# Optimization experiments

Hardware: AMD Instinct MI355X
Metric: run time of the kernel (lower is better)

The kernel has to match this reference:

```python
import jax, jax.numpy as jnp
import numpy as np

N, M, D = 2048, 50000, 128


def setup_inputs() -> dict:
    key = jax.random.key(0)
    kz, kr = jax.random.split(key)
    z = jax.random.normal(kz, (N, D), dtype=jnp.float32)
    ref = jax.random.normal(kr, (M, D), dtype=jnp.float32)  # stands in for the concatenated in_dl batches
    return {"z": z, "ref": ref, "k": 10}


def reference(z, ref, k):
    # L2-normalize rows (matches z / z.norm(dim=1, keepdim=True))
    zn = z / jnp.linalg.norm(z, axis=1, keepdims=True)      # [N, D]
    rn = ref / jnp.linalg.norm(ref, axis=1, keepdims=True)  # [M, D]
    # Pairwise L2 distances via ||a||^2 + ||b||^2 - 2 a.b (same math as the
    # broadcast (rep_batch - rep_z).norm(dim=2), without the O(N*M*D) blowup).
    sq = (jnp.sum(zn * zn, axis=1)[:, None]
          + jnp.sum(rn * rn, axis=1)[None, :]
          - 2.0 * jnp.einsum('nd,md->nm', zn, rn))          # [N, M]
    dist = jnp.sqrt(jnp.maximum(sq, 1e-12))
    # Full sort along the reference axis, take the k-th smallest distance.
    return jnp.sort(dist, axis=1)[:, k]                      # [N]
```

## Files before the change

kernel.cpp:

```cpp
#include <hip/hip_runtime.h>


#define D_DIM 128
#define TQB 256
#define BR 64
#define NCH 64
#define NSUB (NCH * 32)
#define KK 11
#define NCAND 32
#define SLOTS 26
#define DNF 2816

typedef __bf16 bf16_t;
typedef bf16_t bf16x8 __attribute__((ext_vector_type(8)));
typedef float f32x16 __attribute__((ext_vector_type(16)));

__device__ __forceinline__ unsigned short f2bf(float f) {
    unsigned u = __float_as_uint(f);
    return (unsigned short)((u + 0x7fffu + ((u >> 16) & 1u)) >> 16);
}

__global__ __launch_bounds__(256) void normalize_bf16(
    const float* __restrict__ z, const float* __restrict__ ref,
    unsigned short* __restrict__ zb, unsigned short* __restrict__ rb,
    int N, int M)
{
    const int w = threadIdx.x >> 6;
    const int l = threadIdx.x & 63;
    const int row = blockIdx.x * 4 + w;
    if (row >= N + M) return;
    const float* in; unsigned short* out; int r;
    if (row < N) { in = z;   out = zb; r = row; }
    else         { in = ref; out = rb; r = row - N; }
    const float2 v = ((const float2*)in)[(size_t)r * 64 + l];
    float ss = v.x * v.x + v.y * v.y;
    #pragma unroll
    for (int off = 32; off > 0; off >>= 1) ss += __shfl_xor(ss, off);
    const float inv = rsqrtf(ss);
    ushort2 o; o.x = f2bf(v.x * inv); o.y = f2bf(v.y * inv);
    ((ushort2*)out)[(size_t)r * 64 + l] = o;
}

__device__ __forceinline__ void gld_lds16(const unsigned short* g,
                                          unsigned short* l) {
    __builtin_amdgcn_global_load_lds(
        (__attribute__((address_space(1))) void*)g,
        (__attribute__((address_space(3))) void*)l, 16, 0, 0);
}

__global__ __launch_bounds__(512) void knn_maxes(
    const unsigned short* __restrict__ zb, const unsigned short* __restrict__ rb,
    float* __restrict__ maxes, int N, int M, int chunk)
{
    __shared__ __align__(16) unsigned short Bt[2 * BR * D_DIM];

    const int nwg = 8 * NCH;
    const int bid = (int)blockIdx.x + 8 * (int)blockIdx.y;
    const int swz = (bid & 7) * (nwg >> 3) + (bid >> 3);
    const int bx = swz & 7;
    const int by = swz >> 3;

    const int t = threadIdx.x;
    const int lane = t & 63;
    const int w = t >> 6;
    const int quad = lane >> 4;
    const int ln = lane & 15;
    const int l31 = lane & 31;
    const int hi = lane >> 5;
    const int row = bx * TQB + w * 32 + l31;
    const int c0 = by * chunk;
    const int c1 = min(c0 + chunk, M);
    const int clen = c1 - c0;
    const int nt = (clen + BR - 1) / BR;

    bf16x8 qfr[8];
    #pragma unroll
    for (int ks = 0; ks < 8; ++ks)
        qfr[ks] = *(const bf16x8*)&zb[(size_t)row * D_DIM + ks * 16 + hi * 8];

    float mx[16];
    #pragma unroll
    for (int r = 0; r < 16; ++r) mx[r] = -3.0f;

    auto stage = [&](int half, int tile) {
        const int s0 = c0 + tile * BR;
        #pragma unroll
        for (int i = 0; i < 2; ++i) {
            const int r = w * 8 + i * 4 + quad;
            int g = s0 + r; if (g > M - 1) g = M - 1;
            const int sl = ln ^ (r & 15);
            gld_lds16(&rb[(size_t)g * D_DIM + sl * 8],
                      &Bt[half * (BR * D_DIM) + (w * 8 + i * 4) * D_DIM]);
        }
    };

    stage(0, 0);
    stage(1, nt > 1 ? 1 : 0);

    for (int it = 0; it < nt; ++it) {
        if (it + 1 < nt) asm volatile("s_waitcnt vmcnt(2)" ::: "memory");
        else             asm volatile("s_waitcnt vmcnt(0)" ::: "memory");
        __builtin_amdgcn_s_barrier();
        asm volatile("" ::: "memory");
        __builtin_amdgcn_sched_barrier(0);

        const int cur = it & 1;
        const unsigned short* Bc = &Bt[cur * (BR * D_DIM)];

        f32x16 acc0 = {0,0,0,0,0,0,0,0,0,0,0,0,0,0,0,0};
        f32x16 acc1 = {0,0,0,0,0,0,0,0,0,0,0,0,0,0,0,0};

        __builtin_amdgcn_s_setprio(1);
        #pragma unroll
        for (int ks = 0; ks < 8; ++ks) {
            const int sl = ((ks * 2 + hi) ^ ln) * 8;
            bf16x8 a0 = *(const bf16x8*)&Bc[(l31)      * D_DIM + sl];
            bf16x8 a1 = *(const bf16x8*)&Bc[(32 + l31) * D_DIM + sl];
            acc0 = __builtin_amdgcn_mfma_f32_32x32x16_bf16(a0, qfr[ks], acc0, 0, 0, 0);
            acc1 = __builtin_amdgcn_mfma_f32_32x32x16_bf16(a1, qfr[ks], acc1, 0, 0, 0);
        }
        __builtin_amdgcn_s_setprio(0);

        const int rem = clen - it * BR;
        if (rem >= BR) {
            #pragma unroll
            for (int r = 0; r < 16; ++r)
                mx[r] = fmaxf(mx[r], fmaxf(acc0[r], acc1[r]));
        } else {
            #pragma unroll
            for (int r = 0; r < 16; ++r) {
                const int crow = (r & 3) + 8 * (r >> 2) + 4 * hi;
                if (crow < rem)      mx[r] = fmaxf(mx[r], acc0[r]);
                if (32 + crow < rem) mx[r] = fmaxf(mx[r], acc1[r]);
            }
        }

        __builtin_amdgcn_sched_barrier(0);
        asm volatile("" ::: "memory");
        __builtin_amdgcn_s_barrier();
        if (it + 2 < nt) stage(cur, it + 2);
    }

    float* mp = &maxes[(size_t)row * NSUB + by * 32 + hi * 16];
    #pragma unroll
    for (int r4 = 0; r4 < 4; ++r4) {
        float4 v4 = { mx[r4 * 4], mx[r4 * 4 + 1], mx[r4 * 4 + 2], mx[r4 * 4 + 3] };
        *(float4*)&mp[r4 * 4] = v4;
    }
}

__device__ __forceinline__ float kth_largest_64(float* s, int kk, int t) {
    float cur = -3.0f;
    for (int it = 0; it <= kk; ++it) {
        float m = s[0];
        #pragma unroll
        for (int off = 32; off > 0; off >>= 1) m = fmaxf(m, __shfl_xor(m, off));
        cur = m;
        unsigned long long b = __ballot(s[0] == m);
        bool owner = ((int)(__ffsll(b) - 1) == t);
        #pragma unroll
        for (int j = 0; j < KK - 1; ++j) s[j] = owner ? s[j + 1] : s[j];
        if (owner) s[KK - 1] = -3.0f;
    }
    return cur;
}

__global__ __launch_bounds__(256) void knn_select(
    const unsigned short* __restrict__ zb, const unsigned short* __restrict__ rb,
    const float* __restrict__ maxes, const int* __restrict__ kp,
    float* __restrict__ out, int M, int chunk)
{
    const int row = blockIdx.x;
    const int t = threadIdx.x;
    __shared__ float dbuf[DNF];
    __shared__ int cand_s[NCAND];
    __shared__ int cn_s;

    const int kk = *kp;
    if (t == 0) cn_s = 0;

    if (t < 64) {
        float s[KK];
        #pragma unroll
        for (int j = 0; j < KK; ++j) s[j] = -3.0f;
        #pragma unroll
        for (int i = 0; i < NSUB / 64; ++i) {
            float v = maxes[(size_t)row * NSUB + t + 64 * i];
            #pragma unroll
            for (int j = 0; j < KK; ++j) {
                float hi = fmaxf(s[j], v), lo = fminf(s[j], v);
                s[j] = hi; v = lo;
            }
        }
        const float T = kth_largest_64(s, kk, t);
        #pragma unroll
        for (int i = 0; i < NSUB / 64; ++i) {
            float v = maxes[(size_t)row * NSUB + t + 64 * i];
            if (v >= T) {
                int sl = atomicAdd(&cn_s, 1);
                if (sl < NCAND) cand_s[sl] = t + 64 * i;
            }
        }
    }

    const int gl = t & 7;
    const int grp = t >> 3;
    float q0r[8], q1r[8];
    {
        bf16x8 qv0 = *(const bf16x8*)&zb[(size_t)row * D_DIM + gl * 8];
        bf16x8 qv1 = *(const bf16x8*)&zb[(size_t)row * D_DIM + 64 + gl * 8];
        #pragma unroll
        for (int e = 0; e < 8; ++e) { q0r[e] = (float)qv0[e]; q1r[e] = (float)qv1[e]; }
    }
    __syncthreads();

    const int cn = cn_s;
    const int slots = ((chunk + 63) >> 6) * 2;
    int nsel;

    if (cn <= NCAND && slots <= SLOTS) {
        const int W = cn * slots;
        for (int i = t; i < W; i += 256) dbuf[i] = -3.0f;
        __syncthreads();
        for (int ci = 0; ci < cn; ++ci) {
            const int s  = cand_s[ci];
            const int by = s >> 5;
            const int h2 = (s >> 4) & 1;
            const int r  = s & 15;
            const int base = (r & 3) + 8 * (r >> 2) + 4 * h2;
            const int c0 = by * chunk;
            const int c1 = min(c0 + chunk, M);
            for (int sl = grp; sl < slots; sl += 32) {
                const int ref = c0 + (sl >> 1) * 64 + (sl & 1) * 32 + base;
                const bool valid = ref < c1;
                float p = 0.f;
                if (valid) {
                    const unsigned short* rp = &rb[(size_t)ref * D_DIM + gl * 8];
                    bf16x8 r0 = *(const bf16x8*)rp;
                    bf16x8 r1 = *(const bf16x8*)(rp + 64);
                    #pragma unroll
                    for (int e = 0; e < 8; ++e) {
                        p = fmaf((float)r0[e], q0r[e], p);
                        p = fmaf((float)r1[e], q1r[e], p);
                    }
                }
                p += __shfl_xor(p, 1);
                p += __shfl_xor(p, 2);
                p += __shfl_xor(p, 4);
                if (gl == 0 && valid) dbuf[ci * slots + sl] = p;
            }
        }
        nsel = W;
    } else {
        float s[KK];
        #pragma unroll
        for (int j = 0; j < KK; ++j) s[j] = -3.0f;
        for (int g = grp; g < M; g += 32) {
            const unsigned short* rp = &rb[(size_t)g * D_DIM + gl * 8];
            bf16x8 r0 = *(const bf16x8*)rp;
            bf16x8 r1 = *(const bf16x8*)(rp + 64);
            float p = 0.f;
            #pragma unroll
            for (int e = 0; e < 8; ++e) {
                p = fmaf((float)r0[e], q0r[e], p);
                p = fmaf((float)r1[e], q1r[e], p);
            }
            p += __shfl_xor(p, 1);
            p += __shfl_xor(p, 2);
            p += __shfl_xor(p, 4);
            #pragma unroll
            for (int j = 0; j < KK; ++j) {
                float hi = fmaxf(s[j], p), lo = fminf(s[j], p);
                s[j] = hi; p = lo;
            }
        }
        #pragma unroll
        for (int j = 0; j < KK; ++j) dbuf[t * KK + j] = s[j];
        nsel = DNF;
    }
    __syncthreads();

    if (t < 64) {
        float s[KK];
        #pragma unroll
        for (int j = 0; j < KK; ++j) s[j] = -3.0f;
        for (int j = t; j < nsel; j += 64) {
            float v = dbuf[j];
            #pragma unroll
            for (int q = 0; q < KK; ++q) {
                float hi = fmaxf(s[q], v), lo = fminf(s[q], v);
                s[q] = hi; v = lo;
            }
        }
        const float cur = kth_largest_64(s, kk, t);
        if (t == 0) out[row] = sqrtf(fmaxf(2.0f - 2.0f * cur, 1e-12f));
    }
}

extern "C" void kernel_launch(void* const* d_in, const int* in_sizes, int n_in,
                              void* d_out, int out_size, void* d_ws, size_t ws_size,
                              hipStream_t stream) {
    const float* z   = (const float*)d_in[0];
    const float* ref = (const float*)d_in[1];
    const int*   kp  = (const int*)d_in[2];
    float* out = (float*)d_out;

    const int N = in_sizes[0] / D_DIM;
    const int M = in_sizes[1] / D_DIM;

    unsigned short* zbuf = (unsigned short*)d_ws;
    unsigned short* rbuf = zbuf + (size_t)N * D_DIM;
    float* maxes = (float*)(rbuf + (size_t)M * D_DIM);

    normalize_bf16<<<(N + M + 3) / 4, 256, 0, stream>>>(z, ref, zbuf, rbuf, N, M);

    const int chunk = (M + NCH - 1) / NCH;
    dim3 grid(N / TQB, NCH);

    knn_maxes<<<grid, 512, 0, stream>>>(zbuf, rbuf, maxes, N, M, chunk);
    knn_select<<<N, 256, 0, stream>>>(zbuf, rbuf, maxes, kp, out, M, chunk);
}
```

Baseline: 137.4 us.

## Double ref tile to 128 rows and parallelize candidate selection across four waves

The ref tile per pipeline stage in knn_maxes grows from 64 to 128 rows, using four MFMA accumulators per wave and an occupancy hint of two blocks per CU. This halves the number of barrier/wait iterations per chunk at the cost of more LDS and registers. In knn_select, the top-k threshold over the maxes array is now computed by all four waves, each producing a partial top-k that is merged by one wave. The candidate rescoring loop is flattened across candidates and slots, which removes a separate zero-fill pass and keeps the thread groups busy.

```diff
diff --git a/kernel.cpp b/kernel.cpp
--- a/kernel.cpp
+++ b/kernel.cpp
@@ -3,12 +3,12 @@
 
 #define D_DIM 128
 #define TQB 256
-#define BR 64
+#define BR 128
 #define NCH 64
 #define NSUB (NCH * 32)
 #define KK 11
 #define NCAND 32
-#define SLOTS 26
+#define SLOTS 28
 #define DNF 2816
 
 typedef __bf16 bf16_t;
@@ -48,7 +48,7 @@
         (__attribute__((address_space(3))) void*)l, 16, 0, 0);
 }
 
-__global__ __launch_bounds__(512) void knn_maxes(
+__global__ __launch_bounds__(512, 2) void knn_maxes(
     const unsigned short* __restrict__ zb, const unsigned short* __restrict__ rb,
     float* __restrict__ maxes, int N, int M, int chunk)
 {
@@ -85,12 +85,12 @@
     auto stage = [&](int half, int tile) {
         const int s0 = c0 + tile * BR;
         #pragma unroll
-        for (int i = 0; i < 2; ++i) {
-            const int r = w * 8 + i * 4 + quad;
+        for (int i = 0; i < 4; ++i) {
+            const int r = w * 16 + i * 4 + quad;
             int g = s0 + r; if (g > M - 1) g = M - 1;
             const int sl = ln ^ (r & 15);
             gld_lds16(&rb[(size_t)g * D_DIM + sl * 8],
-                      &Bt[half * (BR * D_DIM) + (w * 8 + i * 4) * D_DIM]);
+                      &Bt[half * (BR * D_DIM) + (w * 16 + i * 4) * D_DIM]);
         }
     };
 
@@ -98,7 +98,7 @@
     stage(1, nt > 1 ? 1 : 0);
 
     for (int it = 0; it < nt; ++it) {
-        if (it + 1 < nt) asm volatile("s_waitcnt vmcnt(2)" ::: "memory");
+        if (it + 1 < nt) asm volatile("s_waitcnt vmcnt(4)" ::: "memory");
         else             asm volatile("s_waitcnt vmcnt(0)" ::: "memory");
         __builtin_amdgcn_s_barrier();
         asm volatile("" ::: "memory");
@@ -109,6 +109,8 @@
 
         f32x16 acc0 = {0,0,0,0,0,0,0,0,0,0,0,0,0,0,0,0};
         f32x16 acc1 = {0,0,0,0,0,0,0,0,0,0,0,0,0,0,0,0};
+        f32x16 acc2 = {0,0,0,0,0,0,0,0,0,0,0,0,0,0,0,0};
+        f32x16 acc3 = {0,0,0,0,0,0,0,0,0,0,0,0,0,0,0,0};
 
         __builtin_amdgcn_s_setprio(1);
         #pragma unroll
@@ -116,8 +118,12 @@
             const int sl = ((ks * 2 + hi) ^ ln) * 8;
             bf16x8 a0 = *(const bf16x8*)&Bc[(l31)      * D_DIM + sl];
             bf16x8 a1 = *(const bf16x8*)&Bc[(32 + l31) * D_DIM + sl];
+            bf16x8 a2 = *(const bf16x8*)&Bc[(64 + l31) * D_DIM + sl];
+            bf16x8 a3 = *(const bf16x8*)&Bc[(96 + l31) * D_DIM + sl];
             acc0 = __builtin_amdgcn_mfma_f32_32x32x16_bf16(a0, qfr[ks], acc0, 0, 0, 0);
             acc1 = __builtin_amdgcn_mfma_f32_32x32x16_bf16(a1, qfr[ks], acc1, 0, 0, 0);
+            acc2 = __builtin_amdgcn_mfma_f32_32x32x16_bf16(a2, qfr[ks], acc2, 0, 0, 0);
+            acc3 = __builtin_amdgcn_mfma_f32_32x32x16_bf16(a3, qfr[ks], acc3, 0, 0, 0);
         }
         __builtin_amdgcn_s_setprio(0);
 
@@ -125,13 +131,16 @@
         if (rem >= BR) {
             #pragma unroll
             for (int r = 0; r < 16; ++r)
-                mx[r] = fmaxf(mx[r], fmaxf(acc0[r], acc1[r]));
+                mx[r] = fmaxf(mx[r],
+                         fmaxf(fmaxf(acc0[r], acc1[r]), fmaxf(acc2[r], acc3[r])));
         } else {
             #pragma unroll
             for (int r = 0; r < 16; ++r) {
                 const int crow = (r & 3) + 8 * (r >> 2) + 4 * hi;
                 if (crow < rem)      mx[r] = fmaxf(mx[r], acc0[r]);
                 if (32 + crow < rem) mx[r] = fmaxf(mx[r], acc1[r]);
+                if (64 + crow < rem) mx[r] = fmaxf(mx[r], acc2[r]);
+                if (96 + crow < rem) mx[r] = fmaxf(mx[r], acc3[r]);
             }
         }
 
@@ -149,7 +158,7 @@
     }
 }
 
-__device__ __forceinline__ float kth_largest_64(float* s, int kk, int t) {
+__device__ __forceinline__ float kth_largest_64(float* s, int kk, int lane) {
     float cur = -3.0f;
     for (int it = 0; it <= kk; ++it) {
         float m = s[0];
@@ -157,12 +166,27 @@
         for (int off = 32; off > 0; off >>= 1) m = fmaxf(m, __shfl_xor(m, off));
         cur = m;
         unsigned long long b = __ballot(s[0] == m);
-        bool owner = ((int)(__ffsll(b) - 1) == t);
+        bool owner = ((int)(__ffsll(b) - 1) == lane);
         #pragma unroll
         for (int j = 0; j < KK - 1; ++j) s[j] = owner ? s[j + 1] : s[j];
         if (owner) s[KK - 1] = -3.0f;
     }
     return cur;
+}
+
+__device__ __forceinline__ void wave_topk_to_lds(float* s, int kk, int lane,
+                                                 float* dst) {
+    for (int it = 0; it <= kk; ++it) {
+        float m = s[0];
+        #pragma unroll
+        for (int off = 32; off > 0; off >>= 1) m = fmaxf(m, __shfl_xor(m, off));
+        if (lane == 0) dst[it] = m;
+        unsigned long long b = __ballot(s[0] == m);
+        bool owner = ((int)(__ffsll(b) - 1) == lane);
+        #pragma unroll
+        for (int j = 0; j < KK - 1; ++j) s[j] = owner ? s[j + 1] : s[j];
+        if (owner) s[KK - 1] = -3.0f;
+    }
 }
 
 __global__ __launch_bounds__(256) void knn_select(
@@ -172,35 +196,31 @@
 {
     const int row = blockIdx.x;
     const int t = threadIdx.x;
+    const int lane = t & 63;
+    const int wv = t >> 6;
     __shared__ float dbuf[DNF];
+    __shared__ float tops[4 * KK];
+    __shared__ float T_s;
     __shared__ int cand_s[NCAND];
     __shared__ int cn_s;
 
     const int kk = *kp;
     if (t == 0) cn_s = 0;
 
-    if (t < 64) {
+    {
         float s[KK];
         #pragma unroll
         for (int j = 0; j < KK; ++j) s[j] = -3.0f;
         #pragma unroll
-        for (int i = 0; i < NSUB / 64; ++i) {
-            float v = maxes[(size_t)row * NSUB + t + 64 * i];
+        for (int i = 0; i < NSUB / 256; ++i) {
+            float v = maxes[(size_t)row * NSUB + wv * (NSUB / 4) + lane + 64 * i];
             #pragma unroll
             for (int j = 0; j < KK; ++j) {
                 float hi = fmaxf(s[j], v), lo = fminf(s[j], v);
                 s[j] = hi; v = lo;
             }
         }
-        const float T = kth_largest_64(s, kk, t);
-        #pragma unroll
-        for (int i = 0; i < NSUB / 64; ++i) {
-            float v = maxes[(size_t)row * NSUB + t + 64 * i];
-            if (v >= T) {
-                int sl = atomicAdd(&cn_s, 1);
-                if (sl < NCAND) cand_s[sl] = t + 64 * i;
-            }
-        }
+        wave_topk_to_lds(s, kk, lane, &tops[wv * KK]);
     }
 
     const int gl = t & 7;
@@ -214,15 +234,39 @@
     }
     __syncthreads();
 
+    if (t < 64) {
+        float s[KK];
+        s[0] = (t < 4 * (kk + 1)) ? tops[t] : -3.0f;
+        #pragma unroll
+        for (int j = 1; j < KK; ++j) s[j] = -3.0f;
+        const float T = kth_largest_64(s, kk, lane);
+        if (t == 0) T_s = T;
+    }
+    __syncthreads();
+
+    {
+        const float T = T_s;
+        #pragma unroll
+        for (int i = 0; i < NSUB / 256; ++i) {
+            int idx = wv * (NSUB / 4) + lane + 64 * i;
+            float v = maxes[(size_t)row * NSUB + idx];
+            if (v >= T) {
+                int sl = atomicAdd(&cn_s, 1);
+                if (sl < NCAND) cand_s[sl] = idx;
+            }
+        }
+    }
+    __syncthreads();
+
     const int cn = cn_s;
-    const int slots = ((chunk + 63) >> 6) * 2;
+    const int slots = ((chunk + BR - 1) / BR) * 4;
     int nsel;
 
     if (cn <= NCAND && slots <= SLOTS) {
         const int W = cn * slots;
-        for (int i = t; i < W; i += 256) dbuf[i] = -3.0f;
-        __syncthreads();
-        for (int ci = 0; ci < cn; ++ci) {
+        int ci = grp / slots;
+        int sl = grp - ci * slots;
+        for (int gs = grp; gs < W; gs += 32) {
             const int s  = cand_s[ci];
             const int by = s >> 5;
             const int h2 = (s >> 4) & 1;
@@ -230,25 +274,25 @@
             const int base = (r & 3) + 8 * (r >> 2) + 4 * h2;
             const int c0 = by * chunk;
             const int c1 = min(c0 + chunk, M);
-            for (int sl = grp; sl < slots; sl += 32) {
-                const int ref = c0 + (sl >> 1) * 64 + (sl & 1) * 32 + base;
-                const bool valid = ref < c1;
-                float p = 0.f;
-                if (valid) {
-                    const unsigned short* rp = &rb[(size_t)ref * D_DIM + gl * 8];
-                    bf16x8 r0 = *(const bf16x8*)rp;
-                    bf16x8 r1 = *(const bf16x8*)(rp + 64);
-                    #pragma unroll
-                    for (int e = 0; e < 8; ++e) {
-                        p = fmaf((float)r0[e], q0r[e], p);
-                        p = fmaf((float)r1[e], q1r[e], p);
-                    }
+            const int ref = c0 + (sl >> 2) * BR + (sl & 3) * 32 + base;
+            const bool valid = ref < c1;
+            float p = 0.f;
+            if (valid) {
+                const unsigned short* rp = &rb[(size_t)ref * D_DIM + gl * 8];
+                bf16x8 r0 = *(const bf16x8*)rp;
+                bf16x8 r1 = *(const bf16x8*)(rp + 64);
+                #pragma unroll
+                for (int e = 0; e < 8; ++e) {
+                    p = fmaf((float)r0[e], q0r[e], p);
+                    p = fmaf((float)r1[e], q1r[e], p);
                 }
-                p += __shfl_xor(p, 1);
-                p += __shfl_xor(p, 2);
-                p += __shfl_xor(p, 4);
-                if (gl == 0 && valid) dbuf[ci * slots + sl] = p;
-            }
+            }
+            p += __shfl_xor(p, 1);
+            p += __shfl_xor(p, 2);
+            p += __shfl_xor(p, 4);
+            if (gl == 0) dbuf[gs] = valid ? p : -3.0f;
+            sl += 32;
+            while (sl >= slots) { sl -= slots; ++ci; }
         }
         nsel = W;
     } else {
@@ -292,7 +336,7 @@
                 s[q] = hi; v = lo;
             }
         }
-        const float cur = kth_largest_64(s, kk, t);
+        const float cur = kth_largest_64(s, kk, lane);
         if (t == 0) out[row] = sqrtf(fmaxf(2.0f - 2.0f * cur, 1e-12f));
     }
 }
```

Measured after the change: 146.3 us. 1.07x slower.
